# Kernel tuning notes

Measured on AMD Instinct MI355X. Metric: run time of the kernel, lower is better.

The kernel has to match this reference:

```python
import jax, jax.numpy as jnp
import numpy as np

B, N_LATENT, N_NUISANCE, N_OUT = 2048, 64, 16, 2048


def setup_inputs() -> dict:
    key = jax.random.key(0)
    ks = jax.random.split(key, 6)
    z = jax.random.normal(ks[0], (B, N_LATENT + N_NUISANCE), dtype=jnp.float32)
    size_factor = jax.random.uniform(ks[1], (B, 1), dtype=jnp.float32) + 0.5
    # nn.Linear(n_latent, n_out, bias=False): store as [L, O] for z0 @ W
    amat_w = jax.random.normal(ks[2], (N_LATENT, N_OUT), dtype=jnp.float32) / np.sqrt(N_LATENT).astype(np.float32)
    amat_site = jax.random.normal(ks[3], (N_NUISANCE, N_LATENT, N_OUT), dtype=jnp.float32)
    offsets = jax.random.normal(ks[4], (N_NUISANCE, N_OUT), dtype=jnp.float32)
    px_r = jax.random.normal(ks[5], (N_OUT,), dtype=jnp.float32)
    return {"z": z, "size_factor": size_factor, "amat_w": amat_w,
            "amat_site": amat_site, "offsets": offsets, "px_r": px_r}


def reference(z, size_factor, amat_w, amat_site, offsets, px_r):
    n_nuisance = offsets.shape[0]
    nuisance_oh = z[..., -n_nuisance:]          # [B, N] one-hot site indicator
    z0 = z[..., :-n_nuisance]                   # [B, L] latent part
    x1 = z0 @ amat_w                            # [B, O] shared linear decoder
    nuisance_ids = jnp.argmax(nuisance_oh, axis=-1)  # [B] int ids
    # dropout(p=0.1) in eval mode == identity; .detach() -> stop_gradient
    z0_d = jax.lax.stop_gradient(z0)
    As = amat_site[nuisance_ids]                # [B, L, O] per-sample gathered weights
    x2 = jnp.einsum('bl,blo->bo', z0_d, As)     # batched matvec reduction over L
    mu = jax.nn.softmax(x1 + x2 + offsets[nuisance_ids], axis=-1)  # [B, O]
    mu = mu * size_factor                       # scale by per-cell size factor
    theta = jnp.exp(px_r)                       # NB inverse-dispersion, [O]
    return mu, theta
```

## Files before the change

kernel.cpp:

```cpp
#include <hip/hip_runtime.h>
#include <hip/hip_bf16.h>

#define NB 2048
#define NL 64
#define NN 16
#define NROW 80
#define NO 2048
#define TPB 256
#define OPT 8

typedef unsigned int   u32;
typedef unsigned short u16;

__device__ __forceinline__ float bflo(u32 u) { union { u32 i; float f; } c; c.i = u << 16;          return c.f; }
__device__ __forceinline__ float bfhi(u32 u) { union { u32 i; float f; } c; c.i = u & 0xffff0000u;  return c.f; }
__device__ __forceinline__ u16 f2bf(float f) { __hip_bfloat16 h = __float2bfloat16(f); return *(u16*)&h; }

__global__ __launch_bounds__(TPB) void build_m(const float* __restrict__ W,
                                               const float* __restrict__ A,
                                               u16* __restrict__ M) {
    size_t t    = (size_t)blockIdx.x * TPB + threadIdx.x;
    size_t base = t * 4;
    float4 w = *(const float4*)(W + (base & (size_t)(NL * NO - 1)));
    float4 a = *(const float4*)(A + base);
    ushort4 m;
    m.x = f2bf(w.x + a.x);
    m.y = f2bf(w.y + a.y);
    m.z = f2bf(w.z + a.z);
    m.w = f2bf(w.w + a.w);
    *(ushort4*)(M + base) = m;
}

__global__ __launch_bounds__(TPB) void decoder_m(
    const float* __restrict__ z,
    const float* __restrict__ sf,
    const u16*   __restrict__ M,
    const float* __restrict__ offs,
    const float* __restrict__ pxr,
    float* __restrict__ out)
{
    const int b   = blockIdx.x;
    const int tid = threadIdx.x;

    if (b == NB) {
        for (int o = tid; o < NO; o += TPB)
            out[(size_t)NB * NO + o] = __expf(pxr[o]);
        return;
    }

    __shared__ float z0s[NL];
    __shared__ int   s_id;
    __shared__ float s_red[6];

    if (tid < NL) z0s[tid] = z[b * NROW + tid];
    if (tid == 0) {
        float best = -1e30f; int bi = 0;
        for (int i = 0; i < NN; ++i) {
            float v = z[b * NROW + NL + i];
            if (v > best) { best = v; bi = i; }
        }
        s_id = bi;
    }
    __syncthreads();
    const int id = s_id;

    const int o0 = tid * OPT;
    const uint4* mv = (const uint4*)(M + (size_t)id * NL * NO + o0);

    float acc[OPT];
    {
        float4 oa = *(const float4*)(offs + id * NO + o0);
        float4 ob = *(const float4*)(offs + id * NO + o0 + 4);
        acc[0] = oa.x; acc[1] = oa.y; acc[2] = oa.z; acc[3] = oa.w;
        acc[4] = ob.x; acc[5] = ob.y; acc[6] = ob.z; acc[7] = ob.w;
    }

    #pragma unroll 8
    for (int l = 0; l < NL; ++l) {
        const float zl = z0s[l];
        uint4 m = mv[l * (NO / OPT)];
        acc[0] += zl * bflo(m.x); acc[1] += zl * bfhi(m.x);
        acc[2] += zl * bflo(m.y); acc[3] += zl * bfhi(m.y);
        acc[4] += zl * bflo(m.z); acc[5] += zl * bfhi(m.z);
        acc[6] += zl * bflo(m.w); acc[7] += zl * bfhi(m.w);
    }

    float m = acc[0];
    #pragma unroll
    for (int j = 1; j < OPT; ++j) m = fmaxf(m, acc[j]);
    #pragma unroll
    for (int off = 32; off > 0; off >>= 1) m = fmaxf(m, __shfl_down(m, off));
    if ((tid & 63) == 0) s_red[tid >> 6] = m;
    __syncthreads();
    if (tid == 0) s_red[4] = fmaxf(fmaxf(s_red[0], s_red[1]), fmaxf(s_red[2], s_red[3]));
    __syncthreads();
    const float mx = s_red[4];

    float ex[OPT];
    float s = 0.f;
    #pragma unroll
    for (int j = 0; j < OPT; ++j) { ex[j] = __expf(acc[j] - mx); s += ex[j]; }
    #pragma unroll
    for (int off = 32; off > 0; off >>= 1) s += __shfl_down(s, off);
    if ((tid & 63) == 0) s_red[tid >> 6] = s;
    __syncthreads();
    if (tid == 0) s_red[5] = (s_red[0] + s_red[1]) + (s_red[2] + s_red[3]);
    __syncthreads();
    const float scale = sf[b] / s_red[5];

    float* op = out + (size_t)b * NO + o0;
    *(float4*)(op)     = make_float4(ex[0] * scale, ex[1] * scale, ex[2] * scale, ex[3] * scale);
    *(float4*)(op + 4) = make_float4(ex[4] * scale, ex[5] * scale, ex[6] * scale, ex[7] * scale);
}

__global__ __launch_bounds__(TPB) void decoder_f(
    const float* __restrict__ z, const float* __restrict__ sf,
    const float* __restrict__ W, const float* __restrict__ A,
    const float* __restrict__ offs, const float* __restrict__ pxr,
    float* __restrict__ out)
{
    const int b   = blockIdx.x;
    const int tid = threadIdx.x;
    if (b == NB) {
        for (int o = tid; o < NO; o += TPB)
            out[(size_t)NB * NO + o] = __expf(pxr[o]);
        return;
    }
    __shared__ float z0s[NL];
    __shared__ int   s_id;
    __shared__ float s_red[6];
    if (tid < NL) z0s[tid] = z[b * NROW + tid];
    if (tid == 0) {
        float best = -1e30f; int bi = 0;
        for (int i = 0; i < NN; ++i) {
            float v = z[b * NROW + NL + i];
            if (v > best) { best = v; bi = i; }
        }
        s_id = bi;
    }
    __syncthreads();
    const int id = s_id;
    const int o0 = tid * OPT;
    const float* wp = W + o0;
    const float* ap = A + (size_t)id * NL * NO + o0;
    float acc[OPT];
    {
        float4 oa = *(const float4*)(offs + id * NO + o0);
        float4 ob = *(const float4*)(offs + id * NO + o0 + 4);
        acc[0] = oa.x; acc[1] = oa.y; acc[2] = oa.z; acc[3] = oa.w;
        acc[4] = ob.x; acc[5] = ob.y; acc[6] = ob.z; acc[7] = ob.w;
    }
    #pragma unroll 4
    for (int l = 0; l < NL; ++l) {
        const float zl = z0s[l];
        float4 w0 = *(const float4*)(wp + l * NO);
        float4 w1 = *(const float4*)(wp + l * NO + 4);
        float4 a0 = *(const float4*)(ap + l * NO);
        float4 a1 = *(const float4*)(ap + l * NO + 4);
        acc[0] += zl * (w0.x + a0.x); acc[1] += zl * (w0.y + a0.y);
        acc[2] += zl * (w0.z + a0.z); acc[3] += zl * (w0.w + a0.w);
        acc[4] += zl * (w1.x + a1.x); acc[5] += zl * (w1.y + a1.y);
        acc[6] += zl * (w1.z + a1.z); acc[7] += zl * (w1.w + a1.w);
    }
    float m = acc[0];
    #pragma unroll
    for (int j = 1; j < OPT; ++j) m = fmaxf(m, acc[j]);
    #pragma unroll
    for (int off = 32; off > 0; off >>= 1) m = fmaxf(m, __shfl_down(m, off));
    if ((tid & 63) == 0) s_red[tid >> 6] = m;
    __syncthreads();
    if (tid == 0) s_red[4] = fmaxf(fmaxf(s_red[0], s_red[1]), fmaxf(s_red[2], s_red[3]));
    __syncthreads();
    const float mx = s_red[4];
    float ex[OPT];
    float s = 0.f;
    #pragma unroll
    for (int j = 0; j < OPT; ++j) { ex[j] = __expf(acc[j] - mx); s += ex[j]; }
    #pragma unroll
    for (int off = 32; off > 0; off >>= 1) s += __shfl_down(s, off);
    if ((tid & 63) == 0) s_red[tid >> 6] = s;
    __syncthreads();
    if (tid == 0) s_red[5] = (s_red[0] + s_red[1]) + (s_red[2] + s_red[3]);
    __syncthreads();
    const float scale = sf[b] / s_red[5];
    float* op = out + (size_t)b * NO + o0;
    *(float4*)(op)     = make_float4(ex[0] * scale, ex[1] * scale, ex[2] * scale, ex[3] * scale);
    *(float4*)(op + 4) = make_float4(ex[4] * scale, ex[5] * scale, ex[6] * scale, ex[7] * scale);
}

extern "C" void kernel_launch(void* const* d_in, const int* in_sizes, int n_in,
                              void* d_out, int out_size, void* d_ws, size_t ws_size,
                              hipStream_t stream) {
    const float* z    = (const float*)d_in[0];
    const float* sf   = (const float*)d_in[1];
    const float* W    = (const float*)d_in[2];
    const float* A    = (const float*)d_in[3];
    const float* offs = (const float*)d_in[4];
    const float* pxr  = (const float*)d_in[5];
    float* out = (float*)d_out;

    const size_t m_bytes = (size_t)NN * NL * NO * sizeof(u16);
    if (ws_size >= m_bytes) {
        u16* M = (u16*)d_ws;
        hipLaunchKernelGGL(build_m, dim3((NN * NL * NO / 4) / TPB), dim3(TPB), 0, stream, W, A, M);
        hipLaunchKernelGGL(decoder_m, dim3(NB + 1), dim3(TPB), 0, stream, z, sf, M, offs, pxr, out);
    } else {
        hipLaunchKernelGGL(decoder_f, dim3(NB + 1), dim3(TPB), 0, stream, z, sf, W, A, offs, pxr, out);
    }
}
```

Measured before the change: 101.9 us.

## Bucket rows by nuisance id and process groups of rows per block

Adds a single-block kernel that computes argmax ids, counting-sorts rows by site, and emits groups of up to 8 rows sharing a site. The decoder then handles one group per block, staging chunks of the bf16 site matrix in shared memory and reusing each loaded weight across 8 rows, which removes redundant per-row weight reads. In exchange it adds a serial single-block bucketing launch on the critical path, a larger register footprint for 64 accumulators per thread, and extra syncs per chunk.

```diff
diff --git a/kernel.cpp b/kernel.cpp
--- a/kernel.cpp
+++ b/kernel.cpp
@@ -8,13 +8,66 @@
 #define NO 2048
 #define TPB 256
 #define OPT 8
+#define RPB 8
+#define LCH 8
+#define MAXG (NB / RPB + NN)
 
 typedef unsigned int   u32;
 typedef unsigned short u16;
 
-__device__ __forceinline__ float bflo(u32 u) { union { u32 i; float f; } c; c.i = u << 16;          return c.f; }
-__device__ __forceinline__ float bfhi(u32 u) { union { u32 i; float f; } c; c.i = u & 0xffff0000u;  return c.f; }
+struct Group { int id; int start; int nr; int pad; };
+
+__device__ __forceinline__ float bflo(u32 u) { union { u32 i; float f; } c; c.i = u << 16;         return c.f; }
+__device__ __forceinline__ float bfhi(u32 u) { union { u32 i; float f; } c; c.i = u & 0xffff0000u; return c.f; }
 __device__ __forceinline__ u16 f2bf(float f) { __hip_bfloat16 h = __float2bfloat16(f); return *(u16*)&h; }
+
+__global__ __launch_bounds__(TPB) void bucket_rows(
+    const float* __restrict__ z, const float* __restrict__ pxr,
+    int* __restrict__ perm, Group* __restrict__ groups, int* __restrict__ n_groups,
+    float* __restrict__ out)
+{
+    __shared__ int cnt[NN], start[NN], cur[NN];
+    const int tid = threadIdx.x;
+    if (tid < NN) cnt[tid] = 0;
+    for (int o = tid; o < NO; o += TPB)
+        out[(size_t)NB * NO + o] = __expf(pxr[o]);
+    __syncthreads();
+
+    int ids[NB / TPB];
+    #pragma unroll
+    for (int k = 0; k < NB / TPB; ++k) {
+        const int row = tid + k * TPB;
+        const float* p = z + (size_t)row * NROW + NL;
+        float best = p[0]; int bi = 0;
+        #pragma unroll
+        for (int i = 1; i < NN; ++i) { float v = p[i]; if (v > best) { best = v; bi = i; } }
+        ids[k] = bi;
+        atomicAdd(&cnt[bi], 1);
+    }
+    __syncthreads();
+    if (tid == 0) {
+        int acc = 0;
+        for (int i = 0; i < NN; ++i) { start[i] = acc; cur[i] = acc; acc += cnt[i]; }
+    }
+    __syncthreads();
+    #pragma unroll
+    for (int k = 0; k < NB / TPB; ++k) {
+        const int row = tid + k * TPB;
+        const int pos = atomicAdd(&cur[ids[k]], 1);
+        perm[pos] = row;
+    }
+    __syncthreads();
+    if (tid == 0) {
+        int g = 0;
+        for (int i = 0; i < NN; ++i) {
+            for (int off = 0; off < cnt[i]; off += RPB) {
+                groups[g].id = i; groups[g].start = start[i] + off;
+                groups[g].nr = min(RPB, cnt[i] - off); groups[g].pad = 0; ++g;
+            }
+        }
+        *n_groups = g;
+    }
+}
 
 __global__ __launch_bounds__(TPB) void build_m(const float* __restrict__ W,
                                                const float* __restrict__ A,
@@ -24,93 +77,111 @@
     float4 w = *(const float4*)(W + (base & (size_t)(NL * NO - 1)));
     float4 a = *(const float4*)(A + base);
     ushort4 m;
-    m.x = f2bf(w.x + a.x);
-    m.y = f2bf(w.y + a.y);
-    m.z = f2bf(w.z + a.z);
-    m.w = f2bf(w.w + a.w);
+    m.x = f2bf(w.x + a.x); m.y = f2bf(w.y + a.y);
+    m.z = f2bf(w.z + a.z); m.w = f2bf(w.w + a.w);
     *(ushort4*)(M + base) = m;
 }
 
-__global__ __launch_bounds__(TPB) void decoder_m(
-    const float* __restrict__ z,
-    const float* __restrict__ sf,
-    const u16*   __restrict__ M,
-    const float* __restrict__ offs,
-    const float* __restrict__ pxr,
-    float* __restrict__ out)
+__global__ __launch_bounds__(TPB) void decoder_g(
+    const float* __restrict__ z, const float* __restrict__ sf,
+    const u16* __restrict__ M, const float* __restrict__ offs,
+    const int* __restrict__ perm, const Group* __restrict__ groups,
+    const int* __restrict__ n_groups, float* __restrict__ out)
 {
-    const int b   = blockIdx.x;
     const int tid = threadIdx.x;
-
-    if (b == NB) {
-        for (int o = tid; o < NO; o += TPB)
-            out[(size_t)NB * NO + o] = __expf(pxr[o]);
-        return;
-    }
-
-    __shared__ float z0s[NL];
-    __shared__ int   s_id;
-    __shared__ float s_red[6];
-
-    if (tid < NL) z0s[tid] = z[b * NROW + tid];
-    if (tid == 0) {
-        float best = -1e30f; int bi = 0;
-        for (int i = 0; i < NN; ++i) {
-            float v = z[b * NROW + NL + i];
-            if (v > best) { best = v; bi = i; }
-        }
-        s_id = bi;
-    }
-    __syncthreads();
-    const int id = s_id;
+    const int g   = blockIdx.x;
+    if (g >= *n_groups) return;
+    const int id     = groups[g].id;
+    const int pstart = groups[g].start;
+    const int nr     = groups[g].nr;
+
+    __shared__ int   rows_s[RPB];
+    __shared__ float zT[NL][RPB];
+    __shared__ u16   Ml[LCH * NO];
+    __shared__ float red[2][4][RPB];
+
+    if (tid < RPB) rows_s[tid] = perm[pstart + (tid < nr ? tid : 0)];
+    __syncthreads();
+
+    {
+        const int l = tid & 63, r0 = tid >> 6;
+        zT[l][r0]     = z[(size_t)rows_s[r0]     * NROW + l];
+        zT[l][r0 + 4] = z[(size_t)rows_s[r0 + 4] * NROW + l];
+    }
 
     const int o0 = tid * OPT;
-    const uint4* mv = (const uint4*)(M + (size_t)id * NL * NO + o0);
-
-    float acc[OPT];
+    float acc[RPB][OPT];
     {
         float4 oa = *(const float4*)(offs + id * NO + o0);
         float4 ob = *(const float4*)(offs + id * NO + o0 + 4);
-        acc[0] = oa.x; acc[1] = oa.y; acc[2] = oa.z; acc[3] = oa.w;
-        acc[4] = ob.x; acc[5] = ob.y; acc[6] = ob.z; acc[7] = ob.w;
-    }
-
-    #pragma unroll 8
-    for (int l = 0; l < NL; ++l) {
-        const float zl = z0s[l];
-        uint4 m = mv[l * (NO / OPT)];
-        acc[0] += zl * bflo(m.x); acc[1] += zl * bfhi(m.x);
-        acc[2] += zl * bflo(m.y); acc[3] += zl * bfhi(m.y);
-        acc[4] += zl * bflo(m.z); acc[5] += zl * bfhi(m.z);
-        acc[6] += zl * bflo(m.w); acc[7] += zl * bfhi(m.w);
-    }
-
-    float m = acc[0];
-    #pragma unroll
-    for (int j = 1; j < OPT; ++j) m = fmaxf(m, acc[j]);
-    #pragma unroll
-    for (int off = 32; off > 0; off >>= 1) m = fmaxf(m, __shfl_down(m, off));
-    if ((tid & 63) == 0) s_red[tid >> 6] = m;
-    __syncthreads();
-    if (tid == 0) s_red[4] = fmaxf(fmaxf(s_red[0], s_red[1]), fmaxf(s_red[2], s_red[3]));
-    __syncthreads();
-    const float mx = s_red[4];
-
-    float ex[OPT];
-    float s = 0.f;
-    #pragma unroll
-    for (int j = 0; j < OPT; ++j) { ex[j] = __expf(acc[j] - mx); s += ex[j]; }
-    #pragma unroll
-    for (int off = 32; off > 0; off >>= 1) s += __shfl_down(s, off);
-    if ((tid & 63) == 0) s_red[tid >> 6] = s;
-    __syncthreads();
-    if (tid == 0) s_red[5] = (s_red[0] + s_red[1]) + (s_red[2] + s_red[3]);
-    __syncthreads();
-    const float scale = sf[b] / s_red[5];
-
-    float* op = out + (size_t)b * NO + o0;
-    *(float4*)(op)     = make_float4(ex[0] * scale, ex[1] * scale, ex[2] * scale, ex[3] * scale);
-    *(float4*)(op + 4) = make_float4(ex[4] * scale, ex[5] * scale, ex[6] * scale, ex[7] * scale);
+        float offv[OPT] = { oa.x, oa.y, oa.z, oa.w, ob.x, ob.y, ob.z, ob.w };
+        #pragma unroll
+        for (int r = 0; r < RPB; ++r)
+            #pragma unroll
+            for (int c = 0; c < OPT; ++c) acc[r][c] = offv[c];
+    }
+
+    const uint4* Mg  = (const uint4*)(M + (size_t)id * NL * NO);
+    uint4*       Mlv = (uint4*)Ml;
+
+    for (int ch = 0; ch < NL / LCH; ++ch) {
+        __syncthreads();
+        const uint4* src = Mg + ch * LCH * (NO / 8);
+        #pragma unroll
+        for (int j = 0; j < (LCH * NO / 8) / TPB; ++j)
+            Mlv[j * TPB + tid] = src[j * TPB + tid];
+        __syncthreads();
+        #pragma unroll
+        for (int l = 0; l < LCH; ++l) {
+            uint4 m = *(const uint4*)(Ml + l * NO + o0);
+            float v[OPT] = { bflo(m.x), bfhi(m.x), bflo(m.y), bfhi(m.y),
+                             bflo(m.z), bfhi(m.z), bflo(m.w), bfhi(m.w) };
+            const int gl = ch * LCH + l;
+            #pragma unroll
+            for (int r = 0; r < RPB; ++r) {
+                const float zl = zT[gl][r];
+                #pragma unroll
+                for (int c = 0; c < OPT; ++c) acc[r][c] += zl * v[c];
+            }
+        }
+    }
+
+    #pragma unroll
+    for (int r = 0; r < RPB; ++r) {
+        float m = acc[r][0];
+        #pragma unroll
+        for (int c = 1; c < OPT; ++c) m = fmaxf(m, acc[r][c]);
+        #pragma unroll
+        for (int off = 32; off > 0; off >>= 1) m = fmaxf(m, __shfl_down(m, off));
+        if ((tid & 63) == 0) red[0][tid >> 6][r] = m;
+    }
+    __syncthreads();
+    if (tid < RPB)
+        red[0][0][tid] = fmaxf(fmaxf(red[0][0][tid], red[0][1][tid]),
+                               fmaxf(red[0][2][tid], red[0][3][tid]));
+    __syncthreads();
+
+    #pragma unroll
+    for (int r = 0; r < RPB; ++r) {
+        const float mxr = red[0][0][r];
+        float s = 0.f;
+        #pragma unroll
+        for (int c = 0; c < OPT; ++c) { acc[r][c] = __expf(acc[r][c] - mxr); s += acc[r][c]; }
+        #pragma unroll
+        for (int off = 32; off > 0; off >>= 1) s += __shfl_down(s, off);
+        if ((tid & 63) == 0) red[1][tid >> 6][r] = s;
+    }
+    __syncthreads();
+    if (tid < RPB)
+        red[1][0][tid] = (red[1][0][tid] + red[1][1][tid]) + (red[1][2][tid] + red[1][3][tid]);
+    __syncthreads();
+
+    for (int r = 0; r < nr; ++r) {
+        const float scl = sf[rows_s[r]] / red[1][0][r];
+        float* op = out + (size_t)rows_s[r] * NO + o0;
+        *(float4*)(op)     = make_float4(acc[r][0] * scl, acc[r][1] * scl, acc[r][2] * scl, acc[r][3] * scl);
+        *(float4*)(op + 4) = make_float4(acc[r][4] * scl, acc[r][5] * scl, acc[r][6] * scl, acc[r][7] * scl);
+    }
 }
 
 __global__ __launch_bounds__(TPB) void decoder_f(
@@ -122,8 +193,7 @@
     const int b   = blockIdx.x;
     const int tid = threadIdx.x;
     if (b == NB) {
-        for (int o = tid; o < NO; o += TPB)
-            out[(size_t)NB * NO + o] = __expf(pxr[o]);
+        for (int o = tid; o < NO; o += TPB) out[(size_t)NB * NO + o] = __expf(pxr[o]);
         return;
     }
     __shared__ float z0s[NL];
@@ -132,10 +202,7 @@
     if (tid < NL) z0s[tid] = z[b * NROW + tid];
     if (tid == 0) {
         float best = -1e30f; int bi = 0;
-        for (int i = 0; i < NN; ++i) {
-            float v = z[b * NROW + NL + i];
-            if (v > best) { best = v; bi = i; }
-        }
+        for (int i = 0; i < NN; ++i) { float v = z[b * NROW + NL + i]; if (v > best) { best = v; bi = i; } }
         s_id = bi;
     }
     __syncthreads();
@@ -147,8 +214,8 @@
     {
         float4 oa = *(const float4*)(offs + id * NO + o0);
         float4 ob = *(const float4*)(offs + id * NO + o0 + 4);
-        acc[0] = oa.x; acc[1] = oa.y; acc[2] = oa.z; acc[3] = oa.w;
-        acc[4] = ob.x; acc[5] = ob.y; acc[6] = ob.z; acc[7] = ob.w;
+        acc[0]=oa.x; acc[1]=oa.y; acc[2]=oa.z; acc[3]=oa.w;
+        acc[4]=ob.x; acc[5]=ob.y; acc[6]=ob.z; acc[7]=ob.w;
     }
     #pragma unroll 4
     for (int l = 0; l < NL; ++l) {
@@ -184,8 +251,8 @@
     __syncthreads();
     const float scale = sf[b] / s_red[5];
     float* op = out + (size_t)b * NO + o0;
-    *(float4*)(op)     = make_float4(ex[0] * scale, ex[1] * scale, ex[2] * scale, ex[3] * scale);
-    *(float4*)(op + 4) = make_float4(ex[4] * scale, ex[5] * scale, ex[6] * scale, ex[7] * scale);
+    *(float4*)(op)     = make_float4(ex[0]*scale, ex[1]*scale, ex[2]*scale, ex[3]*scale);
+    *(float4*)(op + 4) = make_float4(ex[4]*scale, ex[5]*scale, ex[6]*scale, ex[7]*scale);
 }
 
 extern "C" void kernel_launch(void* const* d_in, const int* in_sizes, int n_in,
@@ -199,11 +266,17 @@
     const float* pxr  = (const float*)d_in[5];
     float* out = (float*)d_out;
 
-    const size_t m_bytes = (size_t)NN * NL * NO * sizeof(u16);
-    if (ws_size >= m_bytes) {
-        u16* M = (u16*)d_ws;
+    const size_t m_bytes  = (size_t)NN * NL * NO * sizeof(u16);
+    const size_t ws_need  = m_bytes + 8192 + 8192 + 256;
+    if (ws_size >= ws_need) {
+        char* wsb = (char*)d_ws;
+        u16*   M       = (u16*)wsb;
+        int*   perm    = (int*)(wsb + m_bytes);
+        Group* groups  = (Group*)(wsb + m_bytes + 8192);
+        int*   ngroups = (int*)(wsb + m_bytes + 8192 + 8192);
+        hipLaunchKernelGGL(bucket_rows, dim3(1), dim3(TPB), 0, stream, z, pxr, perm, groups, ngroups, out);
         hipLaunchKernelGGL(build_m, dim3((NN * NL * NO / 4) / TPB), dim3(TPB), 0, stream, W, A, M);
-        hipLaunchKernelGGL(decoder_m, dim3(NB + 1), dim3(TPB), 0, stream, z, sf, M, offs, pxr, out);
+        hipLaunchKernelGGL(decoder_g, dim3(MAXG), dim3(TPB), 0, stream, z, sf, M, offs, perm, groups, ngroups, out);
     } else {
         hipLaunchKernelGGL(decoder_f, dim3(NB + 1), dim3(TPB), 0, stream, z, sf, W, A, offs, pxr, out);
     }
```

Result: slower. 152.8 us (+50.0%).

## Bucket rows by nuisance site and tile logits GEMM across rows

Applied to the files above, without the earlier changes.

Adds a single-block bucketing kernel that groups batch rows by argmax site, then a GEMM kernel that computes logits for 8 same-site rows per block over 512-column tiles, so each bf16 weight load is reused across several rows. Softmax and scaling move into a separate kernel that reads the logits from a workspace buffer. The aim is to cut the per-row refetch of the 256 KB site weight slice. In exchange it adds two launches, a serial single-block bucketing step, and a full fp32 logits round trip through memory.

```diff
diff --git a/kernel.cpp b/kernel.cpp
--- a/kernel.cpp
+++ b/kernel.cpp
@@ -6,88 +6,153 @@
 #define NN 16
 #define NROW 80
 #define NO 2048
-#define TPB 256
-#define OPT 8
+#define RPB 8
+#define MAXG (NB / RPB + NN)
+#define CTILE 512
+#define NCT (NO / CTILE)
 
 typedef unsigned int   u32;
 typedef unsigned short u16;
 
-__device__ __forceinline__ float bflo(u32 u) { union { u32 i; float f; } c; c.i = u << 16;          return c.f; }
-__device__ __forceinline__ float bfhi(u32 u) { union { u32 i; float f; } c; c.i = u & 0xffff0000u;  return c.f; }
+struct Group { int id; int start; int nr; int pad; };
+
+__device__ __forceinline__ float bflo(u32 u) { union { u32 i; float f; } c; c.i = u << 16;         return c.f; }
+__device__ __forceinline__ float bfhi(u32 u) { union { u32 i; float f; } c; c.i = u & 0xffff0000u; return c.f; }
 __device__ __forceinline__ u16 f2bf(float f) { __hip_bfloat16 h = __float2bfloat16(f); return *(u16*)&h; }
 
-__global__ __launch_bounds__(TPB) void build_m(const float* __restrict__ W,
+__global__ __launch_bounds__(1024) void bucket_all(
+    const float* __restrict__ z, const float* __restrict__ pxr,
+    int* __restrict__ perm, Group* __restrict__ groups, int* __restrict__ ngroups,
+    float* __restrict__ out)
+{
+    __shared__ int cnt[NN], start_s[NN], cur[NN], gbase[NN];
+    const int tid = threadIdx.x;
+    if (tid < NN) cnt[tid] = 0;
+    for (int o = tid; o < NO; o += 1024)
+        out[(size_t)NB * NO + o] = __expf(pxr[o]);
+    __syncthreads();
+
+    int myid[NB / 1024];
+    #pragma unroll
+    for (int k = 0; k < NB / 1024; ++k) {
+        const int row = tid + k * 1024;
+        const float* p = z + (size_t)row * NROW + NL;
+        float best = p[0]; int bi = 0;
+        #pragma unroll
+        for (int i = 1; i < NN; ++i) { float v = p[i]; if (v > best) { best = v; bi = i; } }
+        myid[k] = bi;
+        atomicAdd(&cnt[bi], 1);
+    }
+    __syncthreads();
+    if (tid == 0) {
+        int acc = 0, g = 0;
+        for (int i = 0; i < NN; ++i) {
+            start_s[i] = acc; cur[i] = acc; gbase[i] = g;
+            acc += cnt[i]; g += (cnt[i] + RPB - 1) / RPB;
+        }
+        *ngroups = g;
+    }
+    __syncthreads();
+    #pragma unroll
+    for (int k = 0; k < NB / 1024; ++k) {
+        const int row = tid + k * 1024;
+        const int pos = atomicAdd(&cur[myid[k]], 1);
+        perm[pos] = row;
+    }
+    if (tid < NN) {
+        const int c = cnt[tid], s = start_s[tid], gb = gbase[tid];
+        for (int j = 0; j * RPB < c; ++j) {
+            Group gr; gr.id = tid; gr.start = s + j * RPB;
+            gr.nr = min(RPB, c - j * RPB); gr.pad = 0;
+            groups[gb + j] = gr;
+        }
+    }
+}
+
+__global__ __launch_bounds__(256) void build_m(const float* __restrict__ W,
                                                const float* __restrict__ A,
                                                u16* __restrict__ M) {
-    size_t t    = (size_t)blockIdx.x * TPB + threadIdx.x;
+    size_t t    = (size_t)blockIdx.x * 256 + threadIdx.x;
     size_t base = t * 4;
     float4 w = *(const float4*)(W + (base & (size_t)(NL * NO - 1)));
     float4 a = *(const float4*)(A + base);
     ushort4 m;
-    m.x = f2bf(w.x + a.x);
-    m.y = f2bf(w.y + a.y);
-    m.z = f2bf(w.z + a.z);
-    m.w = f2bf(w.w + a.w);
+    m.x = f2bf(w.x + a.x); m.y = f2bf(w.y + a.y);
+    m.z = f2bf(w.z + a.z); m.w = f2bf(w.w + a.w);
     *(ushort4*)(M + base) = m;
 }
 
-__global__ __launch_bounds__(TPB) void decoder_m(
-    const float* __restrict__ z,
-    const float* __restrict__ sf,
-    const u16*   __restrict__ M,
-    const float* __restrict__ offs,
-    const float* __restrict__ pxr,
-    float* __restrict__ out)
-{
-    const int b   = blockIdx.x;
-    const int tid = threadIdx.x;
-
-    if (b == NB) {
-        for (int o = tid; o < NO; o += TPB)
-            out[(size_t)NB * NO + o] = __expf(pxr[o]);
-        return;
-    }
-
-    __shared__ float z0s[NL];
-    __shared__ int   s_id;
-    __shared__ float s_red[6];
-
-    if (tid < NL) z0s[tid] = z[b * NROW + tid];
-    if (tid == 0) {
-        float best = -1e30f; int bi = 0;
-        for (int i = 0; i < NN; ++i) {
-            float v = z[b * NROW + NL + i];
-            if (v > best) { best = v; bi = i; }
-        }
-        s_id = bi;
-    }
-    __syncthreads();
-    const int id = s_id;
-
-    const int o0 = tid * OPT;
-    const uint4* mv = (const uint4*)(M + (size_t)id * NL * NO + o0);
-
-    float acc[OPT];
+__global__ __launch_bounds__(256) void gemm_logits(
+    const float* __restrict__ z, const u16* __restrict__ M,
+    const float* __restrict__ offs, const int* __restrict__ perm,
+    const Group* __restrict__ groups, const int* __restrict__ ngroups,
+    float* __restrict__ logits)
+{
+    const int g  = blockIdx.x >> 2;
+    const int ct = blockIdx.x & 3;
+    if (g >= *ngroups) return;
+    const int id     = groups[g].id;
+    const int pstart = groups[g].start;
+    const int nr     = groups[g].nr;
+    const int tid    = threadIdx.x;
+
+    __shared__ int   rows_s[RPB];
+    __shared__ float zT[NL][RPB];
+
+    if (tid < RPB) rows_s[tid] = perm[pstart + (tid < nr ? tid : nr - 1)];
+    __syncthreads();
     {
-        float4 oa = *(const float4*)(offs + id * NO + o0);
-        float4 ob = *(const float4*)(offs + id * NO + o0 + 4);
-        acc[0] = oa.x; acc[1] = oa.y; acc[2] = oa.z; acc[3] = oa.w;
-        acc[4] = ob.x; acc[5] = ob.y; acc[6] = ob.z; acc[7] = ob.w;
+        int r = tid >> 6, l = tid & 63;
+        zT[l][r] = z[(size_t)rows_s[r] * NROW + l];
+        int idx2 = tid + 256; r = idx2 >> 6; l = idx2 & 63;
+        zT[l][r] = z[(size_t)rows_s[r] * NROW + l];
+    }
+    __syncthreads();
+
+    const int c0 = ct * CTILE + tid * 2;
+    const u16* Mg = M + (size_t)id * NL * NO + c0;
+
+    float2 acc[RPB];
+    {
+        float2 o2 = *(const float2*)(offs + id * NO + c0);
+        #pragma unroll
+        for (int r = 0; r < RPB; ++r) acc[r] = o2;
     }
 
     #pragma unroll 8
     for (int l = 0; l < NL; ++l) {
-        const float zl = z0s[l];
-        uint4 m = mv[l * (NO / OPT)];
-        acc[0] += zl * bflo(m.x); acc[1] += zl * bfhi(m.x);
-        acc[2] += zl * bflo(m.y); acc[3] += zl * bfhi(m.y);
-        acc[4] += zl * bflo(m.z); acc[5] += zl * bfhi(m.z);
-        acc[6] += zl * bflo(m.w); acc[7] += zl * bfhi(m.w);
-    }
-
-    float m = acc[0];
-    #pragma unroll
-    for (int j = 1; j < OPT; ++j) m = fmaxf(m, acc[j]);
+        u32 m = *(const u32*)(Mg + (size_t)l * NO);
+        float ml = bflo(m), mh = bfhi(m);
+        float4 za = *(const float4*)&zT[l][0];
+        float4 zb = *(const float4*)&zT[l][4];
+        acc[0].x += za.x * ml; acc[0].y += za.x * mh;
+        acc[1].x += za.y * ml; acc[1].y += za.y * mh;
+        acc[2].x += za.z * ml; acc[2].y += za.z * mh;
+        acc[3].x += za.w * ml; acc[3].y += za.w * mh;
+        acc[4].x += zb.x * ml; acc[4].y += zb.x * mh;
+        acc[5].x += zb.y * ml; acc[5].y += zb.y * mh;
+        acc[6].x += zb.z * ml; acc[6].y += zb.z * mh;
+        acc[7].x += zb.w * ml; acc[7].y += zb.w * mh;
+    }
+
+    for (int r = 0; r < nr; ++r)
+        *(float2*)(logits + (size_t)rows_s[r] * NO + c0) = acc[r];
+}
+
+__global__ __launch_bounds__(256) void softmax_scale(
+    const float* __restrict__ logits, const float* __restrict__ sf,
+    float* __restrict__ out)
+{
+    const int b = blockIdx.x, tid = threadIdx.x, o0 = tid * 8;
+    __shared__ float s_red[6];
+
+    const float* lp = logits + (size_t)b * NO + o0;
+    float4 v0 = *(const float4*)lp, v1 = *(const float4*)(lp + 4);
+    float v[8] = { v0.x, v0.y, v0.z, v0.w, v1.x, v1.y, v1.z, v1.w };
+
+    float m = v[0];
+    #pragma unroll
+    for (int j = 1; j < 8; ++j) m = fmaxf(m, v[j]);
     #pragma unroll
     for (int off = 32; off > 0; off >>= 1) m = fmaxf(m, __shfl_down(m, off));
     if ((tid & 63) == 0) s_red[tid >> 6] = m;
@@ -96,24 +161,23 @@
     __syncthreads();
     const float mx = s_red[4];
 
-    float ex[OPT];
     float s = 0.f;
     #pragma unroll
-    for (int j = 0; j < OPT; ++j) { ex[j] = __expf(acc[j] - mx); s += ex[j]; }
+    for (int j = 0; j < 8; ++j) { v[j] = __expf(v[j] - mx); s += v[j]; }
     #pragma unroll
     for (int off = 32; off > 0; off >>= 1) s += __shfl_down(s, off);
     if ((tid & 63) == 0) s_red[tid >> 6] = s;
     __syncthreads();
     if (tid == 0) s_red[5] = (s_red[0] + s_red[1]) + (s_red[2] + s_red[3]);
     __syncthreads();
-    const float scale = sf[b] / s_red[5];
+    const float scl = sf[b] / s_red[5];
 
     float* op = out + (size_t)b * NO + o0;
-    *(float4*)(op)     = make_float4(ex[0] * scale, ex[1] * scale, ex[2] * scale, ex[3] * scale);
-    *(float4*)(op + 4) = make_float4(ex[4] * scale, ex[5] * scale, ex[6] * scale, ex[7] * scale);
-}
-
-__global__ __launch_bounds__(TPB) void decoder_f(
+    *(float4*)(op)     = make_float4(v[0] * scl, v[1] * scl, v[2] * scl, v[3] * scl);
+    *(float4*)(op + 4) = make_float4(v[4] * scl, v[5] * scl, v[6] * scl, v[7] * scl);
+}
+
+__global__ __launch_bounds__(256) void decoder_f(
     const float* __restrict__ z, const float* __restrict__ sf,
     const float* __restrict__ W, const float* __restrict__ A,
     const float* __restrict__ offs, const float* __restrict__ pxr,
@@ -122,8 +186,7 @@
     const int b   = blockIdx.x;
     const int tid = threadIdx.x;
     if (b == NB) {
-        for (int o = tid; o < NO; o += TPB)
-            out[(size_t)NB * NO + o] = __expf(pxr[o]);
+        for (int o = tid; o < NO; o += 256) out[(size_t)NB * NO + o] = __expf(pxr[o]);
         return;
     }
     __shared__ float z0s[NL];
@@ -132,23 +195,20 @@
     if (tid < NL) z0s[tid] = z[b * NROW + tid];
     if (tid == 0) {
         float best = -1e30f; int bi = 0;
-        for (int i = 0; i < NN; ++i) {
-            float v = z[b * NROW + NL + i];
-            if (v > best) { best = v; bi = i; }
-        }
+        for (int i = 0; i < NN; ++i) { float v = z[b * NROW + NL + i]; if (v > best) { best = v; bi = i; } }
         s_id = bi;
     }
     __syncthreads();
     const int id = s_id;
-    const int o0 = tid * OPT;
+    const int o0 = tid * 8;
     const float* wp = W + o0;
     const float* ap = A + (size_t)id * NL * NO + o0;
-    float acc[OPT];
+    float acc[8];
     {
         float4 oa = *(const float4*)(offs + id * NO + o0);
         float4 ob = *(const float4*)(offs + id * NO + o0 + 4);
-        acc[0] = oa.x; acc[1] = oa.y; acc[2] = oa.z; acc[3] = oa.w;
-        acc[4] = ob.x; acc[5] = ob.y; acc[6] = ob.z; acc[7] = ob.w;
+        acc[0]=oa.x; acc[1]=oa.y; acc[2]=oa.z; acc[3]=oa.w;
+        acc[4]=ob.x; acc[5]=ob.y; acc[6]=ob.z; acc[7]=ob.w;
     }
     #pragma unroll 4
     for (int l = 0; l < NL; ++l) {
@@ -164,7 +224,7 @@
     }
     float m = acc[0];
     #pragma unroll
-    for (int j = 1; j < OPT; ++j) m = fmaxf(m, acc[j]);
+    for (int j = 1; j < 8; ++j) m = fmaxf(m, acc[j]);
     #pragma unroll
     for (int off = 32; off > 0; off >>= 1) m = fmaxf(m, __shfl_down(m, off));
     if ((tid & 63) == 0) s_red[tid >> 6] = m;
@@ -172,10 +232,10 @@
     if (tid == 0) s_red[4] = fmaxf(fmaxf(s_red[0], s_red[1]), fmaxf(s_red[2], s_red[3]));
     __syncthreads();
     const float mx = s_red[4];
-    float ex[OPT];
+    float ex[8];
     float s = 0.f;
     #pragma unroll
-    for (int j = 0; j < OPT; ++j) { ex[j] = __expf(acc[j] - mx); s += ex[j]; }
+    for (int j = 0; j < 8; ++j) { ex[j] = __expf(acc[j] - mx); s += ex[j]; }
     #pragma unroll
     for (int off = 32; off > 0; off >>= 1) s += __shfl_down(s, off);
     if ((tid & 63) == 0) s_red[tid >> 6] = s;
@@ -184,8 +244,8 @@
     __syncthreads();
     const float scale = sf[b] / s_red[5];
     float* op = out + (size_t)b * NO + o0;
-    *(float4*)(op)     = make_float4(ex[0] * scale, ex[1] * scale, ex[2] * scale, ex[3] * scale);
-    *(float4*)(op + 4) = make_float4(ex[4] * scale, ex[5] * scale, ex[6] * scale, ex[7] * scale);
+    *(float4*)(op)     = make_float4(ex[0]*scale, ex[1]*scale, ex[2]*scale, ex[3]*scale);
+    *(float4*)(op + 4) = make_float4(ex[4]*scale, ex[5]*scale, ex[6]*scale, ex[7]*scale);
 }
 
 extern "C" void kernel_launch(void* const* d_in, const int* in_sizes, int n_in,
@@ -199,12 +259,22 @@
     const float* pxr  = (const float*)d_in[5];
     float* out = (float*)d_out;
 
-    const size_t m_bytes = (size_t)NN * NL * NO * sizeof(u16);
-    if (ws_size >= m_bytes) {
-        u16* M = (u16*)d_ws;
-        hipLaunchKernelGGL(build_m, dim3((NN * NL * NO / 4) / TPB), dim3(TPB), 0, stream, W, A, M);
-        hipLaunchKernelGGL(decoder_m, dim3(NB + 1), dim3(TPB), 0, stream, z, sf, M, offs, pxr, out);
+    const size_t M_OFF = 0, PERM_OFF = 4u << 20, GRP_OFF = (4u << 20) + 8192,
+                 NG_OFF = (4u << 20) + 16384, LG_OFF = 8u << 20;
+    const size_t ws_need = LG_OFF + (size_t)NB * NO * sizeof(float);
+    if (ws_size >= ws_need) {
+        char* wsb = (char*)d_ws;
+        u16*   M       = (u16*)(wsb + M_OFF);
+        int*   perm    = (int*)(wsb + PERM_OFF);
+        Group* groups  = (Group*)(wsb + GRP_OFF);
+        int*   ngroups = (int*)(wsb + NG_OFF);
+        float* logits  = (float*)(wsb + LG_OFF);
+        hipLaunchKernelGGL(bucket_all, dim3(1), dim3(1024), 0, stream, z, pxr, perm, groups, ngroups, out);
+        hipLaunchKernelGGL(build_m, dim3((NN * NL * NO / 4) / 256), dim3(256), 0, stream, W, A, M);
+        hipLaunchKernelGGL(gemm_logits, dim3(MAXG * NCT), dim3(256), 0, stream,
+                           z, M, offs, perm, groups, ngroups, logits);
+        hipLaunchKernelGGL(softmax_scale, dim3(NB), dim3(256), 0, stream, logits, sf, out);
     } else {
-        hipLaunchKernelGGL(decoder_f, dim3(NB + 1), dim3(TPB), 0, stream, z, sf, W, A, offs, pxr, out);
-    }
-}
+        hipLaunchKernelGGL(decoder_f, dim3(NB + 1), dim3(256), 0, stream, z, sf, W, A, offs, pxr, out);
+    }
+}
```

Measured after the change: 118.5 us. +16.3%, slower.
